# Performance work log

Measured on AMD Instinct MI355X. Metric: run time of the kernel, lower is better.

The kernel has to match this reference:

```python
import jax, jax.numpy as jnp
import numpy as np

S, A, F, D = 512, 128, 128, 6


def setup_inputs() -> dict:
    key = jax.random.key(0)
    k1, k2 = jax.random.split(key)
    atoms = jax.random.normal(k1, (S, A, F), dtype=jnp.float32)
    # edges in [-1, A); -1 marks missing neighbors (padding)
    edges = jax.random.randint(k2, (S, A, D), -1, A, dtype=jnp.int64)
    return {"atoms": atoms, "edges": edges}


def lookup_neighbors(atoms, edges, maskvalue, include_self):
    # atoms: (S, A, F), edges: (S, A, D) with -1 padding
    s, a, f = atoms.shape
    # prepend a masked "null atom" row at index 0; shift edge indices by +1
    null_row = jnp.full((s, 1, f), maskvalue, dtype=atoms.dtype)
    masked_atoms = jnp.concatenate([null_row, atoms], axis=1)  # (S, A+1, F)
    idx = edges + 1  # -1 padding -> 0 (null row)
    if include_self:
        self_idx = jnp.broadcast_to(jnp.arange(1, a + 1, dtype=idx.dtype)[None, :, None], (s, a, 1))
        idx = jnp.concatenate([self_idx, idx], axis=-1)  # (S, A, D+1)
    # gather neighbor features: (S, A, D+1, F)
    batch_idx = jnp.arange(s)[:, None, None]
    return masked_atoms[batch_idx, idx]


def reference(atoms, edges):
    neighbor_feats = lookup_neighbors(atoms, edges, maskvalue=-jnp.inf, include_self=True)
    max_features = neighbor_feats.max(axis=2)  # (S, A, F)
    atom_degrees = (edges != -1).sum(axis=-1, keepdims=True)  # (S, A, 1)
    general_atom_mask = (atom_degrees != 0).astype(atoms.dtype)
    return max_features * general_atom_mask
```

## Files before the change

kernel.cpp:

```cpp
#include <hip/hip_runtime.h>
#include <stdint.h>


constexpr int S  = 512;
constexpr int A  = 128;
constexpr int F  = 128;
constexpr int D  = 6;
constexpr int QF = 32;
constexpr int ROWB = QF * 4;

#define GLOBAL_AS __attribute__((address_space(1)))
#define LDS_AS    __attribute__((address_space(3)))

__global__ __launch_bounds__(256, 8) void graphpool_kernel(
    const float* __restrict__ atoms,
    const int*   __restrict__ edges,
    float*       __restrict__ out)
{
    __shared__ __align__(16) float sl[A * QF];
    __shared__ __align__(16) int   se[A * 8];

    const int tid  = threadIdx.x;
    const int qb   = blockIdx.x & 3;
    const int s    = blockIdx.x >> 2;
    const int wave = tid >> 6;
    const int lane = tid & 63;

    const float* slab = atoms + (size_t)s * (A * F) + qb * QF;
    {
        const int rowq = lane >> 3;
        const int colq = lane & 7;
#pragma unroll
        for (int i = 0; i < 4; ++i) {
            const int chunk = wave * 4 + i;
            const float* gp = slab + (size_t)(chunk * 8 + rowq) * F + colq * 4;
            float* lp = &sl[chunk * 256];
            __builtin_amdgcn_global_load_lds((const GLOBAL_AS float*)gp,
                                             (LDS_AS float*)lp, 16, 0, 0);
        }
    }

    if (tid < A) {
        const int* eg = edges + ((size_t)s * A + tid) * D;
        const int i0 = eg[0], i1 = eg[1], i2 = eg[2];
        const int i3 = eg[3], i4 = eg[4], i5 = eg[5];
        const int deg = (i0 >= 0) + (i1 >= 0) + (i2 >= 0) +
                        (i3 >= 0) + (i4 >= 0) + (i5 >= 0);
        const int self = tid * ROWB;
        int4 w0, w1;
        w0.x = (i0 >= 0) ? i0 * ROWB : self;
        w0.y = (i1 >= 0) ? i1 * ROWB : self;
        w0.z = (i2 >= 0) ? i2 * ROWB : self;
        w0.w = (i3 >= 0) ? i3 * ROWB : self;
        w1.x = (i4 >= 0) ? i4 * ROWB : self;
        w1.y = (i5 >= 0) ? i5 * ROWB : self;
        w1.z = __float_as_int(deg ? 1.0f : 0.0f);
        w1.w = 0;
        *(int4*)&se[tid * 8]     = w0;
        *(int4*)&se[tid * 8 + 4] = w1;
    }

    __syncthreads();

    const int q    = tid & 7;
    const int qoff = q * 16;
    const char* lbase = (const char*)sl;
    float* outb = out + (size_t)s * (A * F) + qb * QF + q * 4;

#pragma unroll
    for (int p = 0; p < 4; ++p) {
        const int a = p * 32 + (tid >> 3);

        const int4 e0 = *(const int4*)&se[a * 8];
        const int4 e1 = *(const int4*)&se[a * 8 + 4];
        const float maskf = __int_as_float(e1.z);

        float4 m = *(const float4*)(lbase + a * ROWB + qoff);
        float4 v;
        v = *(const float4*)(lbase + e0.x + qoff);
        m.x = fmaxf(m.x, v.x); m.y = fmaxf(m.y, v.y);
        m.z = fmaxf(m.z, v.z); m.w = fmaxf(m.w, v.w);
        v = *(const float4*)(lbase + e0.y + qoff);
        m.x = fmaxf(m.x, v.x); m.y = fmaxf(m.y, v.y);
        m.z = fmaxf(m.z, v.z); m.w = fmaxf(m.w, v.w);
        v = *(const float4*)(lbase + e0.z + qoff);
        m.x = fmaxf(m.x, v.x); m.y = fmaxf(m.y, v.y);
        m.z = fmaxf(m.z, v.z); m.w = fmaxf(m.w, v.w);
        v = *(const float4*)(lbase + e0.w + qoff);
        m.x = fmaxf(m.x, v.x); m.y = fmaxf(m.y, v.y);
        m.z = fmaxf(m.z, v.z); m.w = fmaxf(m.w, v.w);
        v = *(const float4*)(lbase + e1.x + qoff);
        m.x = fmaxf(m.x, v.x); m.y = fmaxf(m.y, v.y);
        m.z = fmaxf(m.z, v.z); m.w = fmaxf(m.w, v.w);
        v = *(const float4*)(lbase + e1.y + qoff);
        m.x = fmaxf(m.x, v.x); m.y = fmaxf(m.y, v.y);
        m.z = fmaxf(m.z, v.z); m.w = fmaxf(m.w, v.w);

        m.x *= maskf; m.y *= maskf; m.z *= maskf; m.w *= maskf;

        *(float4*)(outb + (size_t)a * F) = m;
    }
}

extern "C" void kernel_launch(void* const* d_in, const int* in_sizes, int n_in,
                              void* d_out, int out_size, void* d_ws, size_t ws_size,
                              hipStream_t stream) {
    const float* atoms = (const float*)d_in[0];
    const int*   edges = (const int*)d_in[1];
    float*       out   = (float*)d_out;

    graphpool_kernel<<<S * 4, 256, 0, stream>>>(atoms, edges, out);
}
```

Before: 83.88 us.

## Process whole sample per block with double-buffered feature-quarter loads

Each block now covers one sample instead of one feature quarter, using 512 threads, so the neighbor edge table is decoded once per sample rather than four times. The four 32-feature quarters are streamed through two LDS buffers: the next quarter's async global-to-LDS load is issued while the current quarter is max-reduced. In exchange the grid shrinks to 512 larger blocks and a barrier is added per quarter, which may reduce the number of waves available to hide memory latency.

After: 85.91 us. 2.4% more time.

```diff
diff --git a/kernel.cpp b/kernel.cpp
--- a/kernel.cpp
+++ b/kernel.cpp
@@ -8,36 +8,35 @@
 constexpr int D  = 6;
 constexpr int QF = 32;
 constexpr int ROWB = QF * 4;
+constexpr int NT = 512;
 
 #define GLOBAL_AS __attribute__((address_space(1)))
 #define LDS_AS    __attribute__((address_space(3)))
 
-__global__ __launch_bounds__(256, 8) void graphpool_kernel(
+__global__ __launch_bounds__(NT, 4) void graphpool_kernel(
     const float* __restrict__ atoms,
     const int*   __restrict__ edges,
     float*       __restrict__ out)
 {
-    __shared__ __align__(16) float sl[A * QF];
+    __shared__ __align__(16) float sl[2][A * QF];
     __shared__ __align__(16) int   se[A * 8];
 
     const int tid  = threadIdx.x;
-    const int qb   = blockIdx.x & 3;
-    const int s    = blockIdx.x >> 2;
+    const int s    = blockIdx.x;
     const int wave = tid >> 6;
     const int lane = tid & 63;
 
-    const float* slab = atoms + (size_t)s * (A * F) + qb * QF;
-    {
-        const int rowq = lane >> 3;
-        const int colq = lane & 7;
+    const float* sbase = atoms + (size_t)s * (A * F);
+    const int rowq = lane >> 3;
+    const int colq = lane & 7;
+
 #pragma unroll
-        for (int i = 0; i < 4; ++i) {
-            const int chunk = wave * 4 + i;
-            const float* gp = slab + (size_t)(chunk * 8 + rowq) * F + colq * 4;
-            float* lp = &sl[chunk * 256];
-            __builtin_amdgcn_global_load_lds((const GLOBAL_AS float*)gp,
-                                             (LDS_AS float*)lp, 16, 0, 0);
-        }
+    for (int i = 0; i < 2; ++i) {
+        const int chunk = wave * 2 + i;
+        const float* gp = sbase + (size_t)(chunk * 8 + rowq) * F + colq * 4;
+        float* lp = &sl[0][chunk * 256];
+        __builtin_amdgcn_global_load_lds((const GLOBAL_AS float*)gp,
+                                         (LDS_AS float*)lp, 16, 0, 0);
     }
 
     if (tid < A) {
@@ -60,45 +59,62 @@
         *(int4*)&se[tid * 8 + 4] = w1;
     }
 
-    __syncthreads();
-
-    const int q    = tid & 7;
-    const int qoff = q * 16;
-    const char* lbase = (const char*)sl;
-    float* outb = out + (size_t)s * (A * F) + qb * QF + q * 4;
+    const int q8   = tid & 7;
+    const int qoff = q8 * 16;
+    float* orow = out + (size_t)s * (A * F) + q8 * 4;
 
 #pragma unroll
-    for (int p = 0; p < 4; ++p) {
-        const int a = p * 32 + (tid >> 3);
+    for (int q = 0; q < 4; ++q) {
+        __syncthreads();
 
-        const int4 e0 = *(const int4*)&se[a * 8];
-        const int4 e1 = *(const int4*)&se[a * 8 + 4];
-        const float maskf = __int_as_float(e1.z);
+        if (q < 3) {
+            const float* slab = sbase + (size_t)(q + 1) * QF;
+#pragma unroll
+            for (int i = 0; i < 2; ++i) {
+                const int chunk = wave * 2 + i;
+                const float* gp = slab + (size_t)(chunk * 8 + rowq) * F + colq * 4;
+                float* lp = &sl[(q + 1) & 1][chunk * 256];
+                __builtin_amdgcn_global_load_lds((const GLOBAL_AS float*)gp,
+                                                 (LDS_AS float*)lp, 16, 0, 0);
+            }
+        }
 
-        float4 m = *(const float4*)(lbase + a * ROWB + qoff);
-        float4 v;
-        v = *(const float4*)(lbase + e0.x + qoff);
-        m.x = fmaxf(m.x, v.x); m.y = fmaxf(m.y, v.y);
-        m.z = fmaxf(m.z, v.z); m.w = fmaxf(m.w, v.w);
-        v = *(const float4*)(lbase + e0.y + qoff);
-        m.x = fmaxf(m.x, v.x); m.y = fmaxf(m.y, v.y);
-        m.z = fmaxf(m.z, v.z); m.w = fmaxf(m.w, v.w);
-        v = *(const float4*)(lbase + e0.z + qoff);
-        m.x = fmaxf(m.x, v.x); m.y = fmaxf(m.y, v.y);
-        m.z = fmaxf(m.z, v.z); m.w = fmaxf(m.w, v.w);
-        v = *(const float4*)(lbase + e0.w + qoff);
-        m.x = fmaxf(m.x, v.x); m.y = fmaxf(m.y, v.y);
-        m.z = fmaxf(m.z, v.z); m.w = fmaxf(m.w, v.w);
-        v = *(const float4*)(lbase + e1.x + qoff);
-        m.x = fmaxf(m.x, v.x); m.y = fmaxf(m.y, v.y);
-        m.z = fmaxf(m.z, v.z); m.w = fmaxf(m.w, v.w);
-        v = *(const float4*)(lbase + e1.y + qoff);
-        m.x = fmaxf(m.x, v.x); m.y = fmaxf(m.y, v.y);
-        m.z = fmaxf(m.z, v.z); m.w = fmaxf(m.w, v.w);
+        const char* lbase = (const char*)sl[q & 1];
+        float* outq = orow + q * QF;
 
-        m.x *= maskf; m.y *= maskf; m.z *= maskf; m.w *= maskf;
+#pragma unroll
+        for (int p = 0; p < 2; ++p) {
+            const int a = p * 64 + (tid >> 3);
 
-        *(float4*)(outb + (size_t)a * F) = m;
+            const int4 e0 = *(const int4*)&se[a * 8];
+            const int4 e1 = *(const int4*)&se[a * 8 + 4];
+            const float maskf = __int_as_float(e1.z);
+
+            float4 m = *(const float4*)(lbase + a * ROWB + qoff);
+            float4 v;
+            v = *(const float4*)(lbase + e0.x + qoff);
+            m.x = fmaxf(m.x, v.x); m.y = fmaxf(m.y, v.y);
+            m.z = fmaxf(m.z, v.z); m.w = fmaxf(m.w, v.w);
+            v = *(const float4*)(lbase + e0.y + qoff);
+            m.x = fmaxf(m.x, v.x); m.y = fmaxf(m.y, v.y);
+            m.z = fmaxf(m.z, v.z); m.w = fmaxf(m.w, v.w);
+            v = *(const float4*)(lbase + e0.z + qoff);
+            m.x = fmaxf(m.x, v.x); m.y = fmaxf(m.y, v.y);
+            m.z = fmaxf(m.z, v.z); m.w = fmaxf(m.w, v.w);
+            v = *(const float4*)(lbase + e0.w + qoff);
+            m.x = fmaxf(m.x, v.x); m.y = fmaxf(m.y, v.y);
+            m.z = fmaxf(m.z, v.z); m.w = fmaxf(m.w, v.w);
+            v = *(const float4*)(lbase + e1.x + qoff);
+            m.x = fmaxf(m.x, v.x); m.y = fmaxf(m.y, v.y);
+            m.z = fmaxf(m.z, v.z); m.w = fmaxf(m.w, v.w);
+            v = *(const float4*)(lbase + e1.y + qoff);
+            m.x = fmaxf(m.x, v.x); m.y = fmaxf(m.y, v.y);
+            m.z = fmaxf(m.z, v.z); m.w = fmaxf(m.w, v.w);
+
+            m.x *= maskf; m.y *= maskf; m.z *= maskf; m.w *= maskf;
+
+            *(float4*)(outq + (size_t)a * F) = m;
+        }
     }
 }
 
@@ -109,5 +125,5 @@
     const int*   edges = (const int*)d_in[1];
     float*       out   = (float*)d_out;
 
-    graphpool_kernel<<<S * 4, 256, 0, stream>>>(atoms, edges, out);
+    graphpool_kernel<<<S, NT, 0, stream>>>(atoms, edges, out);
 }
```
